# Kernel tuning notes

Measured on AMD Instinct MI355X. Metric: run time of the kernel, lower is better.

Reference implementation:

```python
import jax, jax.numpy as jnp
import numpy as np

B, N, M = 4, 512, 8192
QUERY_DIM, INPUT_DIM = 512, 256
HEADS, DIM_HEAD = 8, 64
ATT_DIM = HEADS * DIM_HEAD  # 512


def setup_inputs() -> dict:
    key = jax.random.key(0)
    ks = jax.random.split(key, 6)
    x = jax.random.normal(ks[0], (B, N, QUERY_DIM), dtype=jnp.float32)
    context = jax.random.normal(ks[1], (B, M, INPUT_DIM), dtype=jnp.float32)
    # Linear weights stored as [in, out] for x @ W
    Wq = jax.random.normal(ks[2], (QUERY_DIM, ATT_DIM), dtype=jnp.float32) / np.sqrt(QUERY_DIM)
    Wkv = jax.random.normal(ks[3], (INPUT_DIM, 2 * ATT_DIM), dtype=jnp.float32) / np.sqrt(INPUT_DIM)
    Wo = jax.random.normal(ks[4], (ATT_DIM, QUERY_DIM), dtype=jnp.float32) / np.sqrt(ATT_DIM)
    bo = jax.random.normal(ks[5], (QUERY_DIM,), dtype=jnp.float32) * 0.01
    return {"x": x, "context": context, "Wq": Wq, "Wkv": Wkv, "Wo": Wo, "bo": bo}


def reference(x, context, Wq, Wkv, Wo, bo):
    scale = DIM_HEAD ** -0.5
    q = x @ Wq                      # [B, N, H*D]
    kv = context @ Wkv              # [B, M, 2*H*D]
    k, v = jnp.split(kv, 2, axis=-1)
    # split heads: b n (h d) -> b h n d
    q = q.reshape(B, N, HEADS, DIM_HEAD).transpose(0, 2, 1, 3)
    k = k.reshape(B, M, HEADS, DIM_HEAD).transpose(0, 2, 1, 3)
    v = v.reshape(B, M, HEADS, DIM_HEAD).transpose(0, 2, 1, 3)
    scores = jnp.einsum('bhid,bhjd->bhij', q, k) * scale  # [B, H, N, M]
    attn = jax.nn.softmax(scores, axis=-1)
    out = jnp.einsum('bhij,bhjd->bhid', attn, v)           # [B, H, N, D]
    out = out.transpose(0, 2, 1, 3).reshape(B, N, ATT_DIM)
    return out @ Wo + bo
```

## Files before the change

kernel.cpp:

```cpp
#include <hip/hip_runtime.h>
#include <hip/hip_bf16.h>
#include <cstdint>

#define NB 4
#define NQ 512
#define NM 8192
#define NH 8
#define DH 64

typedef short bf16x8s __attribute__((ext_vector_type(8)));
typedef short bf16x4s __attribute__((ext_vector_type(4)));
typedef float f32x4  __attribute__((ext_vector_type(4)));

static __device__ __forceinline__ short f2bs(float f) {
    unsigned u = __builtin_bit_cast(unsigned, f);
    return (short)(unsigned short)((u + 0x8000u) >> 16);
}
static __device__ __forceinline__ unsigned pk2(float a, float b) {
    unsigned au = __builtin_bit_cast(unsigned, a) + 0x8000u;
    unsigned bu = __builtin_bit_cast(unsigned, b) + 0x8000u;
    return __builtin_amdgcn_perm(bu, au, 0x07060302u);
}

#if __has_builtin(__builtin_amdgcn_exp2f)
static __device__ __forceinline__ float fexp2(float x) { return __builtin_amdgcn_exp2f(x); }
#else
static __device__ __forceinline__ float fexp2(float x) { return exp2f(x); }
#endif

__global__ __launch_bounds__(256) void prep_weights(
    const float* __restrict__ Wq, const float* __restrict__ Wo,
    const float* __restrict__ Wkv,
    short* __restrict__ Wqf, short* __restrict__ Wof, short* __restrict__ Wkvf)
{
    const int t = threadIdx.x;
    const int w = t >> 6, ln = t & 63;
    const int m16 = ln & 15, quad = ln >> 4;
    int f = blockIdx.x * 4 + w;
    const float* src; short* dst; int N, KS, n0, ks;
    if (f < 512)       { src = Wq;  dst = Wqf;  N = 512;  KS = 16; n0 = f >> 4; ks = f & 15; }
    else if (f < 1024) { f -= 512;  src = Wo;  dst = Wof;  N = 512;  KS = 16; n0 = f >> 4; ks = f & 15; }
    else               { f -= 1024; src = Wkv; dst = Wkvf; N = 1024; KS = 8;  n0 = f >> 3; ks = f & 7; }
    const float* sp = src + (size_t)(ks * 32 + quad * 8) * N + n0 * 16 + m16;
    float v[8];
    #pragma unroll
    for (int j = 0; j < 8; ++j) v[j] = sp[(size_t)j * N];
    uint4 pkv = { pk2(v[0],v[1]), pk2(v[2],v[3]), pk2(v[4],v[5]), pk2(v[6],v[7]) };
    *(uint4*)(dst + ((size_t)(n0 * KS + ks) * 64 + ln) * 8) = pkv;
}

__device__ __forceinline__ void proj32_body(
    const float* __restrict__ A, const short* __restrict__ Wf,
    float* __restrict__ C, const float* __restrict__ bias,
    int tm, int tn, char* smemraw, int t)
{
    short* As = (short*)smemraw;

    const int w = t >> 6, ln = t & 63;
    const int m16 = ln & 15, quad = ln >> 4;
    const int wm = w >> 1, wn = w & 1;

    const int ar = t >> 3, ac = (t & 7) << 3;

    const float* Ap = A + (size_t)(tm * 32 + ar) * 512 + ac;

    f32x4 acc[2] = {};

    {
        float4 a0 = *(const float4*)(Ap);
        float4 a1 = *(const float4*)(Ap + 4);
        uint4 wa = { pk2(a0.x,a0.y), pk2(a0.z,a0.w), pk2(a1.x,a1.y), pk2(a1.z,a1.w) };
        *(uint4*)&As[ar * 72 + ac] = wa;
    }

    #pragma unroll
    for (int k0 = 0; k0 < 512; k0 += 64) {
        short* Ab = As + ((k0 >> 6) & 1) * 2304;
        __syncthreads();

        bf16x8s bfr[2][2];
        #pragma unroll
        for (int ks = 0; ks < 2; ++ks)
            #pragma unroll
            for (int nt = 0; nt < 2; ++nt)
                bfr[ks][nt] = *(const bf16x8s*)(Wf +
                    ((size_t)((tn * 4 + wn * 2 + nt) * 16 + (k0 >> 5) + ks) * 64 + ln) * 8);

        bf16x8s afr[2];
        #pragma unroll
        for (int ks = 0; ks < 2; ++ks)
            afr[ks] = *(const bf16x8s*)&Ab[(wm * 16 + m16) * 72 + ks * 32 + quad * 8];

        float4 a0n, a1n;
        if (k0 + 64 < 512) {
            a0n = *(const float4*)(Ap + k0 + 64);
            a1n = *(const float4*)(Ap + k0 + 68);
        }

        #pragma unroll
        for (int ks = 0; ks < 2; ++ks)
            #pragma unroll
            for (int nt = 0; nt < 2; ++nt)
                acc[nt] = __builtin_amdgcn_mfma_f32_16x16x32_bf16(afr[ks], bfr[ks][nt], acc[nt], 0, 0, 0);

        if (k0 + 64 < 512) {
            short* Abn = As + ((((k0 >> 6) + 1) & 1)) * 2304;
            uint4 wa = { pk2(a0n.x,a0n.y), pk2(a0n.z,a0n.w), pk2(a1n.x,a1n.y), pk2(a1n.z,a1n.w) };
            *(uint4*)&Abn[ar * 72 + ac] = wa;
        }
    }

    const int row0 = tm * 32 + wm * 16 + quad * 4;
    const int col0 = tn * 64 + wn * 32;
    #pragma unroll
    for (int nt = 0; nt < 2; ++nt) {
        const int col = col0 + nt * 16 + m16;
        const float bb = bias ? bias[col] : 0.f;
        #pragma unroll
        for (int r = 0; r < 4; ++r)
            C[(size_t)(row0 + r) * 512 + col] = acc[nt][r] + bb;
    }
}

__device__ __forceinline__ void kv_body(
    const float* __restrict__ A, const short* __restrict__ Wkvf,
    short* __restrict__ Kf, short* __restrict__ Vf,
    int kvid, char* smemraw)
{
    short* As = (short*)smemraw;

    const int t  = threadIdx.x;
    const int tm = ((kvid >> 6) << 3) | (kvid & 7);
    const int tn = (kvid >> 3) & 7;
    const int w  = t >> 6, ln = t & 63;
    const int m16 = ln & 15, quad = ln >> 4;
    const int wm = w & 1, wn = w >> 1;

    const int ar = t >> 3;
    const int ac = (t & 7) << 2;

    const float* Abase = A + (size_t)(tm * 128 + ar) * 256 + ac;

    f32x4 acc[4][4] = {};

    {
        float4 av[4];
        #pragma unroll
        for (int p = 0; p < 4; ++p)
            av[p] = *(const float4*)(Abase + (size_t)p * 32 * 256);
        #pragma unroll
        for (int p = 0; p < 4; ++p) {
            uint2 wv = { pk2(av[p].x, av[p].y), pk2(av[p].z, av[p].w) };
            *(uint2*)&As[(p * 32 + ar) * 40 + ac] = wv;
        }
    }

    #pragma unroll
    for (int k0 = 0; k0 < 256; k0 += 32) {
        short* Ab = As + ((k0 >> 5) & 1) * 5120;
        __syncthreads();

        bf16x8s bfr[4];
        #pragma unroll
        for (int j = 0; j < 4; ++j)
            bfr[j] = *(const bf16x8s*)(Wkvf +
                ((size_t)((tn * 8 + wn * 4 + j) * 8 + (k0 >> 5)) * 64 + ln) * 8);

        bf16x8s af[4];
        #pragma unroll
        for (int i = 0; i < 4; ++i)
            af[i] = *(const bf16x8s*)&Ab[(wm * 64 + i * 16 + m16) * 40 + quad * 8];

        float4 avn[4];
        if (k0 + 32 < 256) {
            #pragma unroll
            for (int p = 0; p < 4; ++p)
                avn[p] = *(const float4*)(Abase + (size_t)p * 32 * 256 + k0 + 32);
        }

        #pragma unroll
        for (int i = 0; i < 4; ++i)
            #pragma unroll
            for (int j = 0; j < 4; ++j)
                acc[i][j] = __builtin_amdgcn_mfma_f32_16x16x32_bf16(af[i], bfr[j], acc[i][j], 0, 0, 0);

        if (k0 + 32 < 256) {
            short* Abn = As + (((k0 >> 5) + 1) & 1) * 5120;
            #pragma unroll
            for (int p = 0; p < 4; ++p) {
                uint2 wv = { pk2(avn[p].x, avn[p].y), pk2(avn[p].z, avn[p].w) };
                *(uint2*)&Abn[(p * 32 + ar) * 40 + ac] = wv;
            }
        }
    }

    const int col0 = tn * 128 + wn * 64;
    const int row0 = tm * 128 + wm * 64;
    const int b    = row0 >> 13;
    const int mr0  = row0 & (NM - 1);

    if (col0 < 512) {
        __syncthreads();
        const int h = col0 >> 6;
        short* Kp = Kf + (size_t)(b * NH + h) * (NM * DH);
        short* S  = (short*)smemraw + w * 2048;
        #pragma unroll
        for (int half = 0; half < 2; ++half) {
            const int i0 = half * 2;
            #pragma unroll
            for (int di = 0; di < 2; ++di)
                #pragma unroll
                for (int j = 0; j < 4; ++j) {
                    const int base = ((quad & 1) * 2 + (j >> 1)) * 512
                                   + (((j & 1) * 2 + (m16 >> 3)) * 16
                                      + (di * 2 + (quad >> 1)) * 4) * 8
                                   + (m16 & 7);
                    #pragma unroll
                    for (int r = 0; r < 4; ++r)
                        S[base + r * 8] = f2bs(acc[i0 + di][j][r]);
                }
            const int gf0 = ((mr0 >> 4) + i0) * 2;
            #pragma unroll
            for (int fl = 0; fl < 4; ++fl) {
                uint4 v = *(const uint4*)&S[fl * 512 + ln * 8];
                *(uint4*)(Kp + ((size_t)(gf0 + fl) * 512 + ln * 8)) = v;
            }
        }
    } else {
        __syncthreads();
        const int h = (col0 - 512) >> 6;
        short* Vp = Vf + (size_t)(b * NH + h) * (NM * DH);
        short* S  = (short*)smemraw + w * 2048;
        #pragma unroll
        for (int half = 0; half < 2; ++half) {
            const int i0 = half * 2;
            #pragma unroll
            for (int di = 0; di < 2; ++di)
                #pragma unroll
                for (int j = 0; j < 4; ++j) {
                    const int base = j * 512 + (di * 2 + (quad >> 1)) * 128
                                   + m16 * 8 + (quad & 1) * 4;
                    #pragma unroll
                    for (int r = 0; r < 4; ++r)
                        S[base + r] = f2bs(acc[i0 + di][j][r]);
                }
            const int g0 = (mr0 >> 5) + half;
            #pragma unroll
            for (int fl = 0; fl < 4; ++fl) {
                uint4 v = *(const uint4*)&S[fl * 512 + ln * 8];
                *(uint4*)(Vp + ((size_t)(fl * 256 + g0) * 64 + ln) * 8) = v;
            }
        }
    }
}

__global__ __launch_bounds__(256) void gemm_kvq(
    const float* __restrict__ x,   const short* __restrict__ Wqf, float* __restrict__ q,
    const float* __restrict__ ctx, const short* __restrict__ Wkvf,
    short* __restrict__ Kf, short* __restrict__ Vf)
{
    __shared__ __align__(16) char smem[20480];
    if (blockIdx.x < 512)
        proj32_body(x, Wqf, q, nullptr, (int)(blockIdx.x >> 3), (int)(blockIdx.x & 7),
                    smem, (int)threadIdx.x);
    else
        kv_body(ctx, Wkvf, Kf, Vf, (int)(blockIdx.x - 512), smem);
}

__global__ __launch_bounds__(256) void gemm_proj32(
    const float* __restrict__ A, const short* __restrict__ Wf,
    float* __restrict__ C, const float* __restrict__ bias)
{
    __shared__ __align__(16) char smem[32 * 72 * 2 * 2];
    proj32_body(A, Wf, C, bias, (int)(blockIdx.x >> 3), (int)(blockIdx.x & 7),
                smem, (int)threadIdx.x);
}

__global__ __launch_bounds__(512, 4) void attn_mfma(
    const float* __restrict__ Q,
    const short* __restrict__ Kfr,
    const short* __restrict__ Vfr,
    float* __restrict__ Og)
{
    __shared__ __align__(16) float Ob[2][32 * 66];
    __shared__ float lbuf[8 * 32];

    const int bid = blockIdx.x;
    const int xcd = bid & 7, g = bid >> 3;
    const int bh  = xcd * 4 + (g & 3);
    const int qt  = g >> 2;
    const int b   = bh >> 3, h = bh & 7;
    const int t   = threadIdx.x;
    const int w   = t >> 6, ln = t & 63;
    const int m16 = ln & 15, quad = ln >> 4;

    const short* Kbase = Kfr + (size_t)bh * (NM * DH);
    const short* Vbase = Vfr + (size_t)bh * (NM * DH);

    const float qsc = 0.125f * 1.44269504f;
    bf16x8s qf[2][2];
    #pragma unroll
    for (int mt = 0; mt < 2; ++mt) {
        const float* qrow = Q + ((size_t)(b * NQ + qt * 32 + mt * 16 + m16)) * 512 + h * 64;
        #pragma unroll
        for (int ks = 0; ks < 2; ++ks) {
            float4 x0 = *(const float4*)(qrow + ks * 32 + quad * 8);
            float4 x1 = *(const float4*)(qrow + ks * 32 + quad * 8 + 4);
            uint4 pkv = { pk2(x0.x * qsc, x0.y * qsc), pk2(x0.z * qsc, x0.w * qsc),
                          pk2(x1.x * qsc, x1.y * qsc), pk2(x1.z * qsc, x1.w * qsc) };
            qf[mt][ks] = *reinterpret_cast<bf16x8s*>(&pkv);
        }
    }

    bf16x8s ones8;
    #pragma unroll
    for (int j = 0; j < 8; ++j) ones8[j] = (short)0x3F80;

    f32x4 o[2][4] = {};
    f32x4 lsum[2] = {};

    bf16x8s kf[4][2];
    {
        const int kc = w * 64;
        #pragma unroll
        for (int nt = 0; nt < 4; ++nt)
            #pragma unroll
            for (int ks = 0; ks < 2; ++ks)
                kf[nt][ks] = *(const bf16x8s*)(Kbase + ((((kc >> 4) + nt) * 2 + ks) << 9) + ln * 8);
    }

    for (int it = 0; it < 16; ++it) {
        const int kc = it * 512 + w * 64;

        bf16x8s va8[4][2];
        #pragma unroll
        for (int dt = 0; dt < 4; ++dt)
            #pragma unroll
            for (int gg = 0; gg < 2; ++gg)
                va8[dt][gg] = *(const bf16x8s*)(Vbase + ((size_t)(dt * 256 + (kc >> 5) + gg) * 64 + ln) * 8);

        f32x4 st[2][4] = {};
        #pragma unroll
        for (int kt = 0; kt < 4; ++kt)
            #pragma unroll
            for (int mt = 0; mt < 2; ++mt) {
                st[mt][kt] = __builtin_amdgcn_mfma_f32_16x16x32_bf16(kf[kt][0], qf[mt][0], st[mt][kt], 0, 0, 0);
                st[mt][kt] = __builtin_amdgcn_mfma_f32_16x16x32_bf16(kf[kt][1], qf[mt][1], st[mt][kt], 0, 0, 0);
            }

        if (it + 1 < 16) {
            const int kn = (it + 1) * 512 + w * 64;
            #pragma unroll
            for (int nt = 0; nt < 4; ++nt)
                #pragma unroll
                for (int ks = 0; ks < 2; ++ks)
                    kf[nt][ks] = *(const bf16x8s*)(Kbase + ((((kn >> 4) + nt) * 2 + ks) << 9) + ln * 8);
        }

        #pragma unroll
        for (int mt = 0; mt < 2; ++mt)
            #pragma unroll
            for (int gg = 0; gg < 2; ++gg) {
                const f32x4 s0 = st[mt][2 * gg];
                const f32x4 s1 = st[mt][2 * gg + 1];
                uint4 pu = { pk2(fexp2(s0[0]), fexp2(s0[1])), pk2(fexp2(s0[2]), fexp2(s0[3])),
                             pk2(fexp2(s1[0]), fexp2(s1[1])), pk2(fexp2(s1[2]), fexp2(s1[3])) };
                bf16x8s pbv = *reinterpret_cast<bf16x8s*>(&pu);
                #pragma unroll
                for (int dt = 0; dt < 4; ++dt)
                    o[mt][dt] = __builtin_amdgcn_mfma_f32_16x16x32_bf16(va8[dt][gg], pbv, o[mt][dt], 0, 0, 0);
                lsum[mt] = __builtin_amdgcn_mfma_f32_16x16x32_bf16(ones8, pbv, lsum[mt], 0, 0, 0);
            }
    }

    if (quad == 0) {
        #pragma unroll
        for (int mt = 0; mt < 2; ++mt)
            lbuf[w * 32 + mt * 16 + m16] = lsum[mt][0];
    }
    if (w < 2) {
        float* dst = Ob[w];
        #pragma unroll
        for (int mt = 0; mt < 2; ++mt)
            #pragma unroll
            for (int dt = 0; dt < 4; ++dt)
                *(f32x4*)&dst[(mt * 16 + m16) * 66 + dt * 16 + quad * 4] = o[mt][dt];
    }
    __syncthreads();
    #pragma unroll
    for (int ph = 1; ph < 4; ++ph) {
        if ((w >> 1) == ph) {
            float* dst = Ob[w & 1];
            #pragma unroll
            for (int mt = 0; mt < 2; ++mt)
                #pragma unroll
                for (int dt = 0; dt < 4; ++dt) {
                    float* p = &dst[(mt * 16 + m16) * 66 + dt * 16 + quad * 4];
                    f32x4 cur = *(f32x4*)p;
                    cur += o[mt][dt];
                    *(f32x4*)p = cur;
                }
        }
        __syncthreads();
    }
    {
        const int row = t >> 4;
        const int d0  = (t & 15) << 2;
        float l = 0.f;
        #pragma unroll
        for (int wi = 0; wi < 8; ++wi) l += lbuf[wi * 32 + row];
        const float inv = 1.0f / l;
        float* op = Og + ((size_t)(b * NQ + qt * 32 + row)) * 512 + h * 64 + d0;
        const int c = row * 66 + d0;
        float4 r;
        r.x = (Ob[0][c + 0] + Ob[1][c + 0]) * inv;
        r.y = (Ob[0][c + 1] + Ob[1][c + 1]) * inv;
        r.z = (Ob[0][c + 2] + Ob[1][c + 2]) * inv;
        r.w = (Ob[0][c + 3] + Ob[1][c + 3]) * inv;
        *(float4*)op = r;
    }
}

extern "C" void kernel_launch(void* const* d_in, const int* in_sizes, int n_in,
                              void* d_out, int out_size, void* d_ws, size_t ws_size,
                              hipStream_t stream) {
    (void)in_sizes; (void)n_in; (void)out_size; (void)ws_size;

    const float* x   = (const float*)d_in[0];
    const float* ctx = (const float*)d_in[1];
    const float* Wq  = (const float*)d_in[2];
    const float* Wkv = (const float*)d_in[3];
    const float* Wo  = (const float*)d_in[4];
    const float* bo  = (const float*)d_in[5];
    float* out = (float*)d_out;

    float* ws    = (float*)d_ws;
    float* q     = ws;
    float* attno = q + (size_t)2048 * 512;
    short* Kf    = (short*)(attno + (size_t)2048 * 512);
    short* Vf    = Kf + (size_t)NB * NH * NM * DH;
    short* Wqf   = Vf + (size_t)NB * NH * NM * DH;
    short* Wof   = Wqf + (size_t)512 * 512;
    short* Wkvf  = Wof + (size_t)512 * 512;

    prep_weights<<<dim3(384), dim3(256), 0, stream>>>(Wq, Wo, Wkv, Wqf, Wof, Wkvf);

    gemm_kvq<<<dim3(2560), dim3(256), 0, stream>>>(x, Wqf, q, ctx, Wkvf, Kf, Vf);

    attn_mfma<<<dim3(512), dim3(512), 0, stream>>>(q, Kf, Vf, attno);

    gemm_proj32<<<dim3(512), dim3(256), 0, stream>>>(attno, Wof, out, bo);
}
```

Baseline: 185.4 us.

## Split KV projection tile across eight waves and pair Q-projection tiles per block

The KV projection block grows to 512 threads. Each wave now computes a 64x32 slice instead of a 64x64 slice, which halves the accumulator registers per wave, and the launch bound is set for four blocks per CU to raise occupancy. The K and V store epilogues are remapped for the new per-wave slices, and two Q-projection tiles now share one 512-thread block, each with its own shared-memory half. In exchange, the A-tile double buffering and register prefetch are removed: each k-step loads, syncs twice and computes serially, so load latency is exposed more.

```diff
diff --git a/kernel.cpp b/kernel.cpp
--- a/kernel.cpp
+++ b/kernel.cpp
@@ -130,141 +130,115 @@
     short* As = (short*)smemraw;
 
     const int t  = threadIdx.x;
-    const int tm = ((kvid >> 6) << 3) | (kvid & 7);
-    const int tn = (kvid >> 3) & 7;
+    const int tm  = ((kvid >> 6) << 3) | (kvid & 7);
+    const int tn0 = (kvid >> 3) & 7;
     const int w  = t >> 6, ln = t & 63;
     const int m16 = ln & 15, quad = ln >> 4;
     const int wm = w & 1, wn = w >> 1;
 
-    const int ar = t >> 3;
-    const int ac = (t & 7) << 2;
+    const int ar = t >> 2;
+    const int ac = (t & 3) << 3;
 
     const float* Abase = A + (size_t)(tm * 128 + ar) * 256 + ac;
 
-    f32x4 acc[4][4] = {};
-
-    {
-        float4 av[4];
-        #pragma unroll
-        for (int p = 0; p < 4; ++p)
-            av[p] = *(const float4*)(Abase + (size_t)p * 32 * 256);
-        #pragma unroll
-        for (int p = 0; p < 4; ++p) {
-            uint2 wv = { pk2(av[p].x, av[p].y), pk2(av[p].z, av[p].w) };
-            *(uint2*)&As[(p * 32 + ar) * 40 + ac] = wv;
-        }
-    }
-
-    #pragma unroll
-    for (int k0 = 0; k0 < 256; k0 += 32) {
-        short* Ab = As + ((k0 >> 5) & 1) * 5120;
+    f32x4 acc[4][2] = {};
+
+    for (int s = 0; s < 8; ++s) {
+        float4 a0 = *(const float4*)(Abase + s * 32);
+        float4 a1 = *(const float4*)(Abase + s * 32 + 4);
         __syncthreads();
-
-        bf16x8s bfr[4];
-        #pragma unroll
-        for (int j = 0; j < 4; ++j)
+        uint4 wa = { pk2(a0.x,a0.y), pk2(a0.z,a0.w), pk2(a1.x,a1.y), pk2(a1.z,a1.w) };
+        *(uint4*)&As[ar * 40 + ac] = wa;
+        __syncthreads();
+
+        bf16x8s bfr[2];
+        #pragma unroll
+        for (int j = 0; j < 2; ++j)
             bfr[j] = *(const bf16x8s*)(Wkvf +
-                ((size_t)((tn * 8 + wn * 4 + j) * 8 + (k0 >> 5)) * 64 + ln) * 8);
-
-        bf16x8s af[4];
-        #pragma unroll
-        for (int i = 0; i < 4; ++i)
-            af[i] = *(const bf16x8s*)&Ab[(wm * 64 + i * 16 + m16) * 40 + quad * 8];
-
-        float4 avn[4];
-        if (k0 + 32 < 256) {
-            #pragma unroll
-            for (int p = 0; p < 4; ++p)
-                avn[p] = *(const float4*)(Abase + (size_t)p * 32 * 256 + k0 + 32);
-        }
-
-        #pragma unroll
-        for (int i = 0; i < 4; ++i)
-            #pragma unroll
-            for (int j = 0; j < 4; ++j)
-                acc[i][j] = __builtin_amdgcn_mfma_f32_16x16x32_bf16(af[i], bfr[j], acc[i][j], 0, 0, 0);
-
-        if (k0 + 32 < 256) {
-            short* Abn = As + (((k0 >> 5) + 1) & 1) * 5120;
-            #pragma unroll
-            for (int p = 0; p < 4; ++p) {
-                uint2 wv = { pk2(avn[p].x, avn[p].y), pk2(avn[p].z, avn[p].w) };
-                *(uint2*)&Abn[(p * 32 + ar) * 40 + ac] = wv;
-            }
-        }
-    }
-
-    const int col0 = tn * 128 + wn * 64;
-    const int row0 = tm * 128 + wm * 64;
+                ((size_t)((tn0 * 8 + wn * 2 + j) * 8 + s) * 64 + ln) * 8);
+
+        #pragma unroll
+        for (int i = 0; i < 4; ++i) {
+            bf16x8s af = *(const bf16x8s*)&As[(wm * 64 + i * 16 + m16) * 40 + quad * 8];
+            acc[i][0] = __builtin_amdgcn_mfma_f32_16x16x32_bf16(af, bfr[0], acc[i][0], 0, 0, 0);
+            acc[i][1] = __builtin_amdgcn_mfma_f32_16x16x32_bf16(af, bfr[1], acc[i][1], 0, 0, 0);
+        }
+    }
+
+    const int row0 = tm * 128;
     const int b    = row0 >> 13;
     const int mr0  = row0 & (NM - 1);
-
-    if (col0 < 512) {
-        __syncthreads();
-        const int h = col0 >> 6;
+    const int g0   = mr0 >> 5;
+
+    __syncthreads();
+    short* S = (short*)smemraw + w * 1024;
+
+    if (tn0 < 4) {
+        const int h = tn0 * 2 + (wn >> 1);
         short* Kp = Kf + (size_t)(b * NH + h) * (NM * DH);
-        short* S  = (short*)smemraw + w * 2048;
-        #pragma unroll
-        for (int half = 0; half < 2; ++half) {
-            const int i0 = half * 2;
-            #pragma unroll
-            for (int di = 0; di < 2; ++di)
+        const int ksel = wn & 1;
+        #pragma unroll
+        for (int hf = 0; hf < 2; ++hf) {
+            #pragma unroll
+            for (int di = 0; di < 2; ++di) {
+                const int i = hf * 2 + di;
                 #pragma unroll
-                for (int j = 0; j < 4; ++j) {
-                    const int base = ((quad & 1) * 2 + (j >> 1)) * 512
-                                   + (((j & 1) * 2 + (m16 >> 3)) * 16
-                                      + (di * 2 + (quad >> 1)) * 4) * 8
-                                   + (m16 & 7);
+                for (int j = 0; j < 2; ++j) {
+                    const int base = (quad & 1) * 512 + (j * 2 + (m16 >> 3)) * 128
+                                   + ((di * 2 + (quad >> 1)) * 4) * 8 + (m16 & 7);
                     #pragma unroll
                     for (int r = 0; r < 4; ++r)
-                        S[base + r * 8] = f2bs(acc[i0 + di][j][r]);
+                        S[base + r * 8] = f2bs(acc[i][j][r]);
                 }
-            const int gf0 = ((mr0 >> 4) + i0) * 2;
-            #pragma unroll
-            for (int fl = 0; fl < 4; ++fl) {
+            }
+            const int g = g0 + wm * 2 + hf;
+            #pragma unroll
+            for (int fl = 0; fl < 2; ++fl) {
                 uint4 v = *(const uint4*)&S[fl * 512 + ln * 8];
-                *(uint4*)(Kp + ((size_t)(gf0 + fl) * 512 + ln * 8)) = v;
+                *(uint4*)(Kp + ((size_t)((g * 2 + fl) * 2 + ksel) * 512 + ln * 8)) = v;
             }
         }
     } else {
-        __syncthreads();
-        const int h = (col0 - 512) >> 6;
+        const int h = (tn0 - 4) * 2 + (wn >> 1);
         short* Vp = Vf + (size_t)(b * NH + h) * (NM * DH);
-        short* S  = (short*)smemraw + w * 2048;
-        #pragma unroll
-        for (int half = 0; half < 2; ++half) {
-            const int i0 = half * 2;
-            #pragma unroll
-            for (int di = 0; di < 2; ++di)
+        #pragma unroll
+        for (int hf = 0; hf < 2; ++hf) {
+            #pragma unroll
+            for (int di = 0; di < 2; ++di) {
+                const int i = hf * 2 + di;
                 #pragma unroll
-                for (int j = 0; j < 4; ++j) {
-                    const int base = j * 512 + (di * 2 + (quad >> 1)) * 128
-                                   + m16 * 8 + (quad & 1) * 4;
+                for (int j = 0; j < 2; ++j) {
+                    const int base = j * 512
+                                   + ((di * 2 + (quad >> 1)) * 16 + m16) * 8
+                                   + (quad & 1) * 4;
                     #pragma unroll
                     for (int r = 0; r < 4; ++r)
-                        S[base + r] = f2bs(acc[i0 + di][j][r]);
+                        S[base + r] = f2bs(acc[i][j][r]);
                 }
-            const int g0 = (mr0 >> 5) + half;
-            #pragma unroll
-            for (int fl = 0; fl < 4; ++fl) {
+            }
+            const int g = g0 + wm * 2 + hf;
+            #pragma unroll
+            for (int fl = 0; fl < 2; ++fl) {
                 uint4 v = *(const uint4*)&S[fl * 512 + ln * 8];
-                *(uint4*)(Vp + ((size_t)(fl * 256 + g0) * 64 + ln) * 8) = v;
-            }
-        }
-    }
-}
-
-__global__ __launch_bounds__(256) void gemm_kvq(
+                *(uint4*)(Vp + ((size_t)((((wn & 1) * 2 + fl) * 256 + g) * 64 + ln) * 8)) = v;
+            }
+        }
+    }
+}
+
+__global__ __launch_bounds__(512, 4) void gemm_kvq(
     const float* __restrict__ x,   const short* __restrict__ Wqf, float* __restrict__ q,
     const float* __restrict__ ctx, const short* __restrict__ Wkvf,
     short* __restrict__ Kf, short* __restrict__ Vf)
 {
-    __shared__ __align__(16) char smem[20480];
-    if (blockIdx.x < 512)
-        proj32_body(x, Wqf, q, nullptr, (int)(blockIdx.x >> 3), (int)(blockIdx.x & 7),
-                    smem, (int)threadIdx.x);
-    else
-        kv_body(ctx, Wkvf, Kf, Vf, (int)(blockIdx.x - 512), smem);
+    __shared__ __align__(16) char smem[18432];
+    if (blockIdx.x < 256) {
+        const int u = (int)(blockIdx.x * 2) + (int)(threadIdx.x >> 8);
+        proj32_body(x, Wqf, q, nullptr, u >> 3, u & 7,
+                    smem + (threadIdx.x >> 8) * 9216, (int)(threadIdx.x & 255));
+    } else {
+        kv_body(ctx, Wkvf, Kf, Vf, (int)(blockIdx.x - 256), smem);
+    }
 }
 
 __global__ __launch_bounds__(256) void gemm_proj32(
@@ -445,7 +419,7 @@
 
     prep_weights<<<dim3(384), dim3(256), 0, stream>>>(Wq, Wo, Wkv, Wqf, Wof, Wkvf);
 
-    gemm_kvq<<<dim3(2560), dim3(256), 0, stream>>>(x, Wqf, q, ctx, Wkvf, Kf, Vf);
+    gemm_kvq<<<dim3(2304), dim3(512), 0, stream>>>(x, Wqf, q, ctx, Wkvf, Kf, Vf);
 
     attn_mfma<<<dim3(512), dim3(512), 0, stream>>>(q, Kf, Vf, attno);
 
```

After: 172.4 us. 7.1% less time.
